# Optimization experiments

Hardware: AMD Instinct MI355X
Metric: run time of the kernel (lower is better)

Reference implementation:

```python
import jax, jax.numpy as jnp
import numpy as np

N_NODES = 100000
N_EDGES = 20000
NNZ = 800000
D_IN = 256
D_OUT = 256


def _segment_mean(feats, seg_ids, num_segments):
    # feats: [nnz, d] gathered features; seg_ids: [nnz] target segment per entry
    s = jax.ops.segment_sum(feats, seg_ids, num_segments=num_segments)
    cnt = jax.ops.segment_sum(jnp.ones((seg_ids.shape[0],), feats.dtype), seg_ids,
                              num_segments=num_segments)
    return s / jnp.maximum(cnt, 1.0)[:, None]


def setup_inputs() -> dict:
    key = jax.random.key(0)
    k1, k2, k3, k4, k5 = jax.random.split(key, 5)
    X = jax.random.normal(k1, (N_NODES, D_IN), dtype=jnp.float32)
    W = jax.random.normal(k2, (D_IN, D_OUT), dtype=jnp.float32) * (1.0 / np.sqrt(D_IN))
    b = jax.random.normal(k3, (D_OUT,), dtype=jnp.float32) * 0.01
    vertex_idx = jax.random.randint(k4, (NNZ,), 0, N_NODES, dtype=jnp.int32)
    edge_idx = jax.random.randint(k5, (NNZ,), 0, N_EDGES, dtype=jnp.int32)
    return {"X": X, "W": W, "b": b, "vertex_idx": vertex_idx, "edge_idx": edge_idx}


def reference(X, W, b, vertex_idx, edge_idx):
    # theta: linear projection
    H = X @ W + b                                   # [N_NODES, D_OUT]
    # v2e mean: hyperedge feature = mean of incident vertex features
    Y = _segment_mean(H[vertex_idx], edge_idx, N_EDGES)   # [N_EDGES, D_OUT]
    # e2v mean: vertex feature = mean of incident hyperedge features
    X_ = _segment_mean(Y[edge_idx], vertex_idx, N_NODES)  # [N_NODES, D_OUT]
    # ReLU; dropout is identity in eval mode
    return jax.nn.relu(X_)
```

## Files before the change

kernel.cpp:

```cpp
#include <hip/hip_runtime.h>
#include <hip/hip_bf16.h>

constexpr int N_NODES = 100000;
constexpr int N_EDGES = 20000;
constexpr int NNZ     = 800000;
constexpr int D       = 256;

typedef unsigned short ushort_t;
typedef unsigned short ushort4v __attribute__((ext_vector_type(4)));
typedef unsigned short ushort8v __attribute__((ext_vector_type(8)));
typedef __bf16         bf16x8   __attribute__((ext_vector_type(8)));
typedef float          f32x4    __attribute__((ext_vector_type(4)));
typedef float          f32x8    __attribute__((ext_vector_type(8)));
typedef unsigned long long u64;
typedef unsigned long long u64x2 __attribute__((ext_vector_type(2)));

static __device__ inline ushort_t f2bf(float f) {
  unsigned u = __builtin_bit_cast(unsigned, f);
  return (ushort_t)((u + 0x7FFFu + ((u >> 16) & 1u)) >> 16);
}

static __device__ inline f32x8 row_f32(const ushort_t* p) {
  bf16x8 b = __builtin_bit_cast(bf16x8, *(const ushort8v*)p);
  return __builtin_convertvector(b, f32x8);
}

static __device__ inline int bsum(u64 x) {
  return (int)((x * 0x0101010101010101ULL) >> 56);
}

constexpr int HCHUNKS   = 32;
constexpr int CHUNK4    = NNZ / 4 / HCHUNKS;
constexpr int PWORDS    = HCHUNKS / 8;
constexpr int NH_RANGES = 5;
constexpr int NH_BINS   = N_NODES / NH_RANGES;
constexpr int NH_BLOCKS = NH_RANGES * HCHUNKS;
constexpr int EH_BLOCKS = HCHUNKS;
constexpr int HIST_BLOCKS  = NH_BLOCKS + EH_BLOCKS;
constexpr int TRANS_BLOCKS = 64;
constexpr int PREP_BLOCKS  = HIST_BLOCKS + TRANS_BLOCKS;
constexpr int HWORDS = 5000;

__global__ __launch_bounds__(256) void prep_kernel(
    const float* __restrict__ W,
    const int* __restrict__ vidx, const int* __restrict__ eidx,
    ushort_t* __restrict__ Wt,
    unsigned char* __restrict__ pe, unsigned char* __restrict__ pn,
    unsigned char* __restrict__ lre, unsigned char* __restrict__ lrn) {
  __shared__ unsigned int hist[HWORDS];
  const int blk = blockIdx.x, tid = threadIdx.x;
  if (blk < HIST_BLOCKS) {
    const bool is_n = blk < NH_BLOCKS;
    const int c  = is_n ? (blk & (HCHUNKS - 1)) : (blk - NH_BLOCKS);
    const int lo = is_n ? (blk >> 5) * NH_BINS : 0;
    const int* __restrict__ idx = is_n ? vidx : eidx;
    unsigned char* __restrict__ lr = is_n ? lrn : lre;
    for (int t = tid; t < HWORDS; t += 256) hist[t] = 0;
    __syncthreads();
    const int base4 = c * CHUNK4;
    for (int k = tid; k < CHUNK4; k += 256) {
      int i4 = base4 + k;
      int4 q = ((const int4*)idx)[i4];
      int vv[4] = {q.x, q.y, q.z, q.w};
#pragma unroll
      for (int j = 0; j < 4; ++j) {
        unsigned rel = (unsigned)(vv[j] - lo);
        if (rel < (unsigned)NH_BINS) {
          unsigned sh = 8u * (rel & 3u);
          unsigned old = atomicAdd(&hist[rel >> 2], 1u << sh);
          lr[(size_t)i4 * 4 + j] = (unsigned char)((old >> sh) & 0xFFu);
        }
      }
    }
    __syncthreads();
    unsigned char* __restrict__ pb = is_n ? pn : pe;
    for (int t = tid; t < NH_BINS; t += 256) {
      unsigned byte = (hist[t >> 2] >> (8u * (t & 3u))) & 0xFFu;
      pb[(size_t)(lo + t) * HCHUNKS + c] = (unsigned char)byte;
    }
  } else {
    int wb = blk - HIST_BLOCKS;
#pragma unroll
    for (int i = 0; i < 4; ++i) {
      int k = wb * 4 + i;
      Wt[(size_t)tid * 256 + k] = f2bf(W[(size_t)k * 256 + tid]);
    }
  }
}

constexpr int SCAN_L    = N_EDGES + N_NODES;
constexpr int SCAN_TPB  = 1024;
constexpr int SCAN_EPT  = 4;
constexpr int SCAN_TILE = SCAN_TPB * SCAN_EPT;
constexpr int SCAN_NB   = (SCAN_L + SCAN_TILE - 1) / SCAN_TILE;

static __device__ inline int bsum32(const u64* P) {
  u64x2 a = *(const u64x2*)P;
  u64x2 b = *(const u64x2*)(P + 2);
  return bsum(a[0]) + bsum(a[1]) + bsum(b[0]) + bsum(b[1]);
}

__global__ __launch_bounds__(1024) void scan_phaseA(
    const u64* __restrict__ pe, const u64* __restrict__ pn,
    int* __restrict__ comb, int* __restrict__ btot) {
  __shared__ int wsum[16];
  const int tid = threadIdx.x, lane = tid & 63, wid = tid >> 6;
  const int base = blockIdx.x * SCAN_TILE + tid * SCAN_EPT;
  int v[SCAN_EPT];
#pragma unroll
  for (int i = 0; i < SCAN_EPT; ++i) {
    int j = base + i;
    int x = 0;
    if (j < SCAN_L)
      x = bsum32(j < N_EDGES ? pe + (size_t)j * PWORDS
                             : pn + (size_t)(j - N_EDGES) * PWORDS);
    v[i] = x;
  }
  int tsum = v[0] + v[1] + v[2] + v[3];
  int x = tsum;
#pragma unroll
  for (int d = 1; d < 64; d <<= 1) {
    int y = __shfl_up(x, (unsigned)d, 64);
    if (lane >= d) x += y;
  }
  if (lane == 63) wsum[wid] = x;
  __syncthreads();
  if (wid == 0) {
    int s = (lane < 16) ? wsum[lane] : 0;
#pragma unroll
    for (int d = 1; d < 16; d <<= 1) {
      int y = __shfl_up(s, (unsigned)d, 64);
      if (lane >= d) s += y;
    }
    if (lane < 16) wsum[lane] = s;
  }
  __syncthreads();
  int texcl = ((wid == 0) ? 0 : wsum[wid - 1]) + (x - tsum);
  int run = texcl;
#pragma unroll
  for (int i = 0; i < SCAN_EPT; ++i) {
    int j = base + i;
    if (j < SCAN_L) comb[j] = run;
    run += v[i];
  }
  if (tid == 0) btot[blockIdx.x] = wsum[15];
}

__global__ __launch_bounds__(1024) void scan_phaseC(
    const int* __restrict__ comb, const int* __restrict__ btot,
    int* __restrict__ eoff, int* __restrict__ noff) {
  int add = 0;
  for (int bdx = 0; bdx < blockIdx.x; ++bdx) add += btot[bdx];
  const int base = blockIdx.x * SCAN_TILE + threadIdx.x * SCAN_EPT;
#pragma unroll
  for (int i = 0; i < SCAN_EPT; ++i) {
    int j = base + i;
    if (j < SCAN_L) {
      int val = comb[j] + add;
      if (j < N_EDGES) eoff[j] = val;
      else             noff[j - N_EDGES] = val - NNZ;
    }
  }
  if (blockIdx.x == 0 && threadIdx.x == 0) {
    eoff[N_EDGES] = NNZ;
    noff[N_NODES] = NNZ;
  }
}

__global__ __launch_bounds__(256) void scatter_calc(
    const int* __restrict__ vidx, const int* __restrict__ eidx,
    const int* __restrict__ eoff, const int* __restrict__ noff,
    const u64* __restrict__ pe, const u64* __restrict__ pn,
    const unsigned char* __restrict__ lre, const unsigned char* __restrict__ lrn,
    int* __restrict__ evals, int* __restrict__ nvals) {
  int i4 = blockIdx.x * 256 + threadIdx.x;
  if (i4 >= NNZ / 4) return;
  int c = i4 / CHUNK4;
  int w = c >> 3, sub = c & 7;
  u64 mw = (1ULL << (8 * sub)) - 1ULL;
  u64 m0 = (w > 0) ? ~0ULL : mw;
  u64 m1 = (w > 1) ? ~0ULL : ((w == 1) ? mw : 0ULL);
  u64 m2 = (w > 2) ? ~0ULL : ((w == 2) ? mw : 0ULL);
  u64 m3 = (w == 3) ? mw : 0ULL;
  int4 e4 = ((const int4*)eidx)[i4];
  int4 v4 = ((const int4*)vidx)[i4];
  unsigned le = *(const unsigned*)(lre + (size_t)i4 * 4);
  unsigned ln = *(const unsigned*)(lrn + (size_t)i4 * 4);
  int ee[4] = {e4.x, e4.y, e4.z, e4.w};
  int vv[4] = {v4.x, v4.y, v4.z, v4.w};
#pragma unroll
  for (int j = 0; j < 4; ++j) {
    int e = ee[j], v = vv[j];
    u64x2 ea = *(const u64x2*)(pe + (size_t)e * PWORDS);
    u64x2 eb = *(const u64x2*)(pe + (size_t)e * PWORDS + 2);
    u64x2 na = *(const u64x2*)(pn + (size_t)v * PWORDS);
    u64x2 nb = *(const u64x2*)(pn + (size_t)v * PWORDS + 2);
    int pre_e = bsum(ea[0] & m0) + bsum(ea[1] & m1) + bsum(eb[0] & m2) + bsum(eb[1] & m3);
    int pre_n = bsum(na[0] & m0) + bsum(na[1] & m1) + bsum(nb[0] & m2) + bsum(nb[1] & m3);
    int re = (int)((le >> (8 * j)) & 0xFFu);
    int rn = (int)((ln >> (8 * j)) & 0xFFu);
    evals[eoff[e] + pre_e + re] = v;
    nvals[noff[v] + pre_n + rn] = e;
  }
}

__global__ __launch_bounds__(256) void gemm_h(
    const float* __restrict__ X, const ushort_t* __restrict__ Wt,
    const float* __restrict__ bias, ushort_t* __restrict__ H) {
  const int w = threadIdx.x >> 6, lane = threadIdx.x & 63;
  const int m15 = lane & 15, q = lane >> 4;
  const int m0 = blockIdx.x * 32 + (w >> 1) * 16;
  const int c0 = (w & 1) * 128;
  const float* xrow = X + (size_t)(m0 + m15) * 256 + q * 8;
  f32x4 acc[8] = { {0,0,0,0}, {0,0,0,0}, {0,0,0,0}, {0,0,0,0},
                   {0,0,0,0}, {0,0,0,0}, {0,0,0,0}, {0,0,0,0} };
  for (int k0 = 0; k0 < 256; k0 += 32) {
    f32x4 xa = *(const f32x4*)(xrow + k0);
    f32x4 xb = *(const f32x4*)(xrow + k0 + 4);
    ushort8v au;
    au[0] = f2bf(xa[0]); au[1] = f2bf(xa[1]); au[2] = f2bf(xa[2]); au[3] = f2bf(xa[3]);
    au[4] = f2bf(xb[0]); au[5] = f2bf(xb[1]); au[6] = f2bf(xb[2]); au[7] = f2bf(xb[3]);
    bf16x8 af = __builtin_bit_cast(bf16x8, au);
#pragma unroll
    for (int t = 0; t < 8; ++t) {
      const ushort_t* brow = Wt + (size_t)(c0 + t * 16 + m15) * 256 + k0 + q * 8;
      bf16x8 bf = __builtin_bit_cast(bf16x8, *(const ushort8v*)brow);
      acc[t] = __builtin_amdgcn_mfma_f32_16x16x32_bf16(af, bf, acc[t], 0, 0, 0);
    }
  }
#pragma unroll
  for (int t = 0; t < 8; ++t) {
    int col = c0 + t * 16 + m15;
    float bv = bias[col];
#pragma unroll
    for (int r = 0; r < 4; ++r) {
      int row = m0 + q * 4 + r;
      H[(size_t)row * 256 + col] = f2bf(acc[t][r] + bv);
    }
  }
}

__global__ __launch_bounds__(256) void v2e_mean(
    const ushort_t* __restrict__ H, const int* __restrict__ eoff,
    const int* __restrict__ evals, ushort_t* __restrict__ Yeb) {
  int half = threadIdx.x >> 5, l32 = threadIdx.x & 31;
  int seg = blockIdx.x * 8 + half;
  int s = eoff[seg], e = eoff[seg + 1];
  const ushort_t* base = H + l32 * 8;
  f32x8 a0 = {0, 0, 0, 0, 0, 0, 0, 0}, a1 = a0, a2 = a0, a3 = a0;
  int j = s;
  for (; j + 3 < e; j += 4) {
    int r0 = evals[j], r1 = evals[j + 1], r2 = evals[j + 2], r3 = evals[j + 3];
    a0 += row_f32(&base[(size_t)r0 * 256]);
    a1 += row_f32(&base[(size_t)r1 * 256]);
    a2 += row_f32(&base[(size_t)r2 * 256]);
    a3 += row_f32(&base[(size_t)r3 * 256]);
  }
  for (; j < e; ++j)
    a0 += row_f32(&base[(size_t)evals[j] * 256]);
  a0 = (a0 + a1) + (a2 + a3);
  float inv = 1.0f / (float)max(e - s, 1);
  ushort8v o;
#pragma unroll
  for (int i = 0; i < 8; ++i) o[i] = f2bf(a0[i] * inv);
  *(ushort8v*)&Yeb[(size_t)seg * 256 + l32 * 8] = o;
}

__global__ __launch_bounds__(256) void e2v_mean_relu(
    const ushort_t* __restrict__ Yeb, const int* __restrict__ noff,
    const int* __restrict__ nvals, float* __restrict__ dst) {
  int half = threadIdx.x >> 5, l32 = threadIdx.x & 31;
  int seg = blockIdx.x * 8 + half;
  int s = noff[seg], e = noff[seg + 1];
  const ushort_t* base = Yeb + l32 * 8;
  f32x8 a0 = {0, 0, 0, 0, 0, 0, 0, 0}, a1 = a0, a2 = a0, a3 = a0;
  int j = s;
  for (; j + 3 < e; j += 4) {
    int r0 = nvals[j], r1 = nvals[j + 1], r2 = nvals[j + 2], r3 = nvals[j + 3];
    a0 += row_f32(&base[(size_t)r0 * 256]);
    a1 += row_f32(&base[(size_t)r1 * 256]);
    a2 += row_f32(&base[(size_t)r2 * 256]);
    a3 += row_f32(&base[(size_t)r3 * 256]);
  }
  for (; j < e; ++j)
    a0 += row_f32(&base[(size_t)nvals[j] * 256]);
  a0 = (a0 + a1) + (a2 + a3);
  float inv = 1.0f / (float)max(e - s, 1);
  float4 o0, o1;
  o0.x = fmaxf(a0[0] * inv, 0.f); o0.y = fmaxf(a0[1] * inv, 0.f);
  o0.z = fmaxf(a0[2] * inv, 0.f); o0.w = fmaxf(a0[3] * inv, 0.f);
  o1.x = fmaxf(a0[4] * inv, 0.f); o1.y = fmaxf(a0[5] * inv, 0.f);
  o1.z = fmaxf(a0[6] * inv, 0.f); o1.w = fmaxf(a0[7] * inv, 0.f);
  size_t b = (size_t)seg * 256 + l32 * 8;
  *(float4*)&dst[b]     = o0;
  *(float4*)&dst[b + 4] = o1;
}

constexpr size_t OFF_H     = 0;
constexpr size_t OFF_YEB   = OFF_H   + (size_t)N_NODES * D * 2;
constexpr size_t OFF_WT    = OFF_YEB + (size_t)N_EDGES * D * 2;
constexpr size_t OFF_PE    = OFF_WT  + (size_t)D * D * 2;
constexpr size_t OFF_PN    = OFF_PE  + (size_t)N_EDGES * HCHUNKS;
constexpr size_t OFF_LRE   = OFF_PN  + (size_t)N_NODES * HCHUNKS;
constexpr size_t OFF_LRN   = OFF_LRE + (size_t)NNZ;
constexpr size_t OFF_EOFF  = OFF_LRN + (size_t)NNZ;
constexpr size_t OFF_NOFF  = OFF_EOFF + (size_t)(N_EDGES + 1 + 3) * 4;
constexpr size_t OFF_EVALS = OFF_NOFF + (size_t)(N_NODES + 1 + 3) * 4;
constexpr size_t OFF_NVALS = OFF_EVALS + (size_t)NNZ * 4;
constexpr size_t OFF_COMB  = OFF_NVALS + (size_t)NNZ * 4;
constexpr size_t OFF_BTOT  = OFF_COMB + (size_t)SCAN_L * 4;

extern "C" void kernel_launch(void* const* d_in, const int* in_sizes, int n_in,
                              void* d_out, int out_size, void* d_ws, size_t ws_size,
                              hipStream_t stream) {
  const float* X    = (const float*)d_in[0];
  const float* W    = (const float*)d_in[1];
  const float* b    = (const float*)d_in[2];
  const int*   vidx = (const int*)d_in[3];
  const int*   eidx = (const int*)d_in[4];
  float*       out  = (float*)d_out;

  char* ws = (char*)d_ws;
  ushort_t* H    = (ushort_t*)(ws + OFF_H);
  ushort_t* Yeb  = (ushort_t*)(ws + OFF_YEB);
  ushort_t* Wt   = (ushort_t*)(ws + OFF_WT);
  unsigned char* pe_b = (unsigned char*)(ws + OFF_PE);
  unsigned char* pn_b = (unsigned char*)(ws + OFF_PN);
  u64* pe_u = (u64*)(ws + OFF_PE);
  u64* pn_u = (u64*)(ws + OFF_PN);
  unsigned char* lre = (unsigned char*)(ws + OFF_LRE);
  unsigned char* lrn = (unsigned char*)(ws + OFF_LRN);
  int* eoff  = (int*)(ws + OFF_EOFF);
  int* noff  = (int*)(ws + OFF_NOFF);
  int* evals = (int*)(ws + OFF_EVALS);
  int* nvals = (int*)(ws + OFF_NVALS);
  int* comb  = (int*)(ws + OFF_COMB);
  int* btot  = (int*)(ws + OFF_BTOT);


  prep_kernel<<<PREP_BLOCKS, 256, 0, stream>>>(W, vidx, eidx, Wt,
                                               pe_b, pn_b, lre, lrn);

  gemm_h<<<N_NODES / 32, 256, 0, stream>>>(X, Wt, b, H);

  scan_phaseA<<<SCAN_NB, SCAN_TPB, 0, stream>>>(pe_u, pn_u, comb, btot);
  scan_phaseC<<<SCAN_NB, SCAN_TPB, 0, stream>>>(comb, btot, eoff, noff);

  scatter_calc<<<(NNZ / 4 + 255) / 256, 256, 0, stream>>>(
      vidx, eidx, eoff, noff, pe_u, pn_u, lre, lrn, evals, nvals);

  v2e_mean<<<N_EDGES / 8, 256, 0, stream>>>(H, eoff, evals, Yeb);

  e2v_mean_relu<<<N_NODES / 8, 256, 0, stream>>>(Yeb, noff, nvals, out);
}
```

Measured before the change: 479.9 us.

## Stage W half in swizzled LDS and run persistent row-tile GEMM blocks

The projection GEMM now launches a fixed grid of 512-thread persistent blocks, each owning one 128-column half of W. Each block loads that half once into LDS with an XOR swizzle to avoid bank conflicts, then loops over 32-row tiles. This removes the repeated global or L2 reads of W that every block did before. In exchange each X row is read and converted to bf16 by two blocks (one per column half), and the 64 KB LDS footprint limits how many blocks fit per CU.

```diff
diff --git a/kernel.cpp b/kernel.cpp
--- a/kernel.cpp
+++ b/kernel.cpp
@@ -204,38 +204,67 @@
   }
 }
 
-__global__ __launch_bounds__(256) void gemm_h(
+constexpr int GEMM_TPB    = 512;
+constexpr int GEMM_RG     = 256;
+constexpr int GEMM_BLOCKS = 2 * GEMM_RG;
+constexpr int ROW_TILES   = N_NODES / 32;
+
+__global__ __launch_bounds__(GEMM_TPB, 4) void gemm_h(
     const float* __restrict__ X, const ushort_t* __restrict__ Wt,
     const float* __restrict__ bias, ushort_t* __restrict__ H) {
-  const int w = threadIdx.x >> 6, lane = threadIdx.x & 63;
+  __shared__ ushort_t blds[128 * 256];
+  const int tid = threadIdx.x;
+  const int chalf = blockIdx.x & 1, rg = blockIdx.x >> 1;
+  {
+    const char* src = (const char*)(Wt + (size_t)chalf * 128 * 256);
+#pragma unroll
+    for (int i = 0; i < 8; ++i) {
+      int o = tid * 16 + i * 8192;
+      ushort8v v = *(const ushort8v*)(src + o);
+      int so = o ^ (((o >> 9) & 7) << 4);
+      *(ushort8v*)((char*)blds + so) = v;
+    }
+  }
+  __syncthreads();
+  const int wid = tid >> 6, lane = tid & 63;
   const int m15 = lane & 15, q = lane >> 4;
-  const int m0 = blockIdx.x * 32 + (w >> 1) * 16;
-  const int c0 = (w & 1) * 128;
-  const float* xrow = X + (size_t)(m0 + m15) * 256 + q * 8;
-  f32x4 acc[8] = { {0,0,0,0}, {0,0,0,0}, {0,0,0,0}, {0,0,0,0},
-                   {0,0,0,0}, {0,0,0,0}, {0,0,0,0}, {0,0,0,0} };
-  for (int k0 = 0; k0 < 256; k0 += 32) {
-    f32x4 xa = *(const f32x4*)(xrow + k0);
-    f32x4 xb = *(const f32x4*)(xrow + k0 + 4);
-    ushort8v au;
-    au[0] = f2bf(xa[0]); au[1] = f2bf(xa[1]); au[2] = f2bf(xa[2]); au[3] = f2bf(xa[3]);
-    au[4] = f2bf(xb[0]); au[5] = f2bf(xb[1]); au[6] = f2bf(xb[2]); au[7] = f2bf(xb[3]);
-    bf16x8 af = __builtin_bit_cast(bf16x8, au);
-#pragma unroll
-    for (int t = 0; t < 8; ++t) {
-      const ushort_t* brow = Wt + (size_t)(c0 + t * 16 + m15) * 256 + k0 + q * 8;
-      bf16x8 bf = __builtin_bit_cast(bf16x8, *(const ushort8v*)brow);
-      acc[t] = __builtin_amdgcn_mfma_f32_16x16x32_bf16(af, bf, acc[t], 0, 0, 0);
-    }
-  }
-#pragma unroll
-  for (int t = 0; t < 8; ++t) {
-    int col = c0 + t * 16 + m15;
-    float bv = bias[col];
+  const int wm = wid & 1, wn = wid >> 1;
+  const int col0 = wn * 32 + m15, col1 = col0 + 16;
+  const int bb0 = col0 * 512 + q * 16, swz0 = (col0 & 7) << 4;
+  const int bb1 = col1 * 512 + q * 16, swz1 = (col1 & 7) << 4;
+  const float bv0 = bias[chalf * 128 + col0];
+  const float bv1 = bias[chalf * 128 + col1];
+
+  for (int tile = rg; tile < ROW_TILES; tile += GEMM_RG) {
+    const float* xrow = X + (size_t)(tile * 32 + wm * 16 + m15) * 256 + q * 8;
+    f32x4 xa[16];
+#pragma unroll
+    for (int i = 0; i < 8; ++i) {
+      xa[2 * i]     = *(const f32x4*)(xrow + i * 32);
+      xa[2 * i + 1] = *(const f32x4*)(xrow + i * 32 + 4);
+    }
+    f32x4 acc0 = {0, 0, 0, 0}, acc1 = {0, 0, 0, 0};
+#pragma unroll
+    for (int ks = 0; ks < 8; ++ks) {
+      ushort8v au;
+#pragma unroll
+      for (int j = 0; j < 4; ++j) {
+        au[j]     = f2bf(xa[2 * ks][j]);
+        au[j + 4] = f2bf(xa[2 * ks + 1][j]);
+      }
+      bf16x8 af = __builtin_bit_cast(bf16x8, au);
+      bf16x8 b0 = __builtin_bit_cast(bf16x8,
+          *(const ushort8v*)((const char*)blds + ((bb0 + ks * 64) ^ swz0)));
+      bf16x8 b1 = __builtin_bit_cast(bf16x8,
+          *(const ushort8v*)((const char*)blds + ((bb1 + ks * 64) ^ swz1)));
+      acc0 = __builtin_amdgcn_mfma_f32_16x16x32_bf16(af, b0, acc0, 0, 0, 0);
+      acc1 = __builtin_amdgcn_mfma_f32_16x16x32_bf16(af, b1, acc1, 0, 0, 0);
+    }
 #pragma unroll
     for (int r = 0; r < 4; ++r) {
-      int row = m0 + q * 4 + r;
-      H[(size_t)row * 256 + col] = f2bf(acc[t][r] + bv);
+      size_t orow = (size_t)(tile * 32 + wm * 16 + q * 4 + r);
+      H[orow * 256 + chalf * 128 + col0] = f2bf(acc0[r] + bv0);
+      H[orow * 256 + chalf * 128 + col1] = f2bf(acc1[r] + bv1);
     }
   }
 }
@@ -341,7 +370,7 @@
   prep_kernel<<<PREP_BLOCKS, 256, 0, stream>>>(W, vidx, eidx, Wt,
                                                pe_b, pn_b, lre, lrn);
 
-  gemm_h<<<N_NODES / 32, 256, 0, stream>>>(X, Wt, b, H);
+  gemm_h<<<GEMM_BLOCKS, GEMM_TPB, 0, stream>>>(X, Wt, b, H);
 
   scan_phaseA<<<SCAN_NB, SCAN_TPB, 0, stream>>>(pe_u, pn_u, comb, btot);
   scan_phaseC<<<SCAN_NB, SCAN_TPB, 0, stream>>>(comb, btot, eoff, noff);
```

New measurement: 462.4 us. 3.6% less time.
